# Performance work log

Measured on AMD Instinct MI355X. Metric: run time of the kernel, lower is better.

Reference implementation:

```python
import jax, jax.numpy as jnp
import numpy as np

G, N, F_IN, H, C = 128, 512, 128, 128, 10
LAMB = 1.0
NEG_SLOPE = 0.2
P_EDGE = 32.0 / N  # avg degree ~32


def setup_inputs() -> dict:
    key = jax.random.key(0)
    ks = jax.random.split(key, 12)
    x = jax.random.normal(ks[0], (G, N, F_IN), dtype=jnp.float32)
    # symmetric 0/1 adjacency without self loops (per-graph dense block)
    a = (jax.random.uniform(ks[1], (G, N, N)) < P_EDGE).astype(jnp.float32)
    adj = jnp.maximum(a, jnp.swapaxes(a, 1, 2)) * (1.0 - jnp.eye(N, dtype=jnp.float32))

    def lin(k, fi, fo):
        return (jax.random.normal(k, (fi, fo), dtype=jnp.float32) / np.float32(np.sqrt(fi)))

    return {
        "x": x, "adj": adj,
        "W1": lin(ks[2], F_IN, H), "b1": jnp.zeros((H,), jnp.float32),
        "W2": lin(ks[3], H, H), "b2": jnp.zeros((H,), jnp.float32),
        "W3": lin(ks[4], H, H), "b3": jnp.zeros((H,), jnp.float32),
        "att1_s": 0.1 * jax.random.normal(ks[5], (H,), dtype=jnp.float32),
        "att1_d": 0.1 * jax.random.normal(ks[6], (H,), dtype=jnp.float32),
        "att2_s": 0.1 * jax.random.normal(ks[7], (H,), dtype=jnp.float32),
        "att2_d": 0.1 * jax.random.normal(ks[8], (H,), dtype=jnp.float32),
        "Wl1": lin(ks[9], 2 * H, H), "bl1": jnp.zeros((H,), jnp.float32),
        "Wl2": lin(ks[10], H, H // 2), "bl2": jnp.zeros((H // 2,), jnp.float32),
        "Wl3": lin(ks[11], H // 2, C), "bl3": jnp.zeros((C,), jnp.float32),
    }


def gcn(x, adj, W, b):
    # GCNConv: D^{-1/2} (A + I) D^{-1/2} X W + b  (self-loop weight 1, edge weights in adj)
    deg = adj.sum(-1) + 1.0                              # [G, n]
    dinv = jax.lax.rsqrt(deg)
    xw = x @ W                                           # [G, n, H]
    agg = jnp.einsum('gij,gjf->gif', adj, dinv[..., None] * xw)
    return dinv[..., None] * agg + (dinv * dinv)[..., None] * xw + b


def info_score(x, adj):
    # HGP-SL node information score: row-wise L1 norm of (I - D^{-1} A) X
    deg = jnp.maximum(adj.sum(-1), 1.0)
    agg = jnp.einsum('gij,gjf->gif', adj, x) / deg[..., None]
    return jnp.sum(jnp.abs(x - agg), axis=-1)            # [G, n]


def hgpsl_pool(x, adj, att_s, att_d, k):
    # top-k node selection by information score, then structure learning:
    # dense (sample=False) path: e_ij = leaky_relu(att.[x_i||x_j]) + lamb*A_ij, softmax over j
    s = info_score(x, adj)
    _, idx = jax.lax.top_k(s, k)                         # [G, k]
    xk = jnp.take_along_axis(x, idx[..., None], axis=1)  # [G, k, H]
    g = jnp.arange(x.shape[0])[:, None, None]
    ak = adj[g, idx[:, :, None], idx[:, None, :]]        # induced adjacency [G, k, k]
    e = jax.nn.leaky_relu((xk @ att_s)[:, :, None] + (xk @ att_d)[:, None, :], NEG_SLOPE)
    attn = jax.nn.softmax(e + LAMB * ak, axis=-1)        # new learned edge weights
    return xk, attn


def readout(x):
    # gmp || gap over nodes
    return jnp.concatenate([x.max(axis=1), x.mean(axis=1)], axis=-1)


def reference(x, adj, W1, b1, W2, b2, W3, b3, att1_s, att1_d, att2_s, att2_d,
              Wl1, bl1, Wl2, bl2, Wl3, bl3):
    h = jax.nn.relu(gcn(x, adj, W1, b1))
    h, a1 = hgpsl_pool(h, adj, att1_s, att1_d, N // 2)
    x1 = readout(h)
    h = jax.nn.relu(gcn(h, a1, W2, b2))
    h, a2 = hgpsl_pool(h, a1, att2_s, att2_d, N // 4)
    x2 = readout(h)
    h = jax.nn.relu(gcn(h, a2, W3, b3))
    x3 = readout(h)
    z = jax.nn.relu(x1) + jax.nn.relu(x2) + jax.nn.relu(x3)
    z = jax.nn.relu(z @ Wl1 + bl1)
    z = jax.nn.relu(z @ Wl2 + bl2)
    return jax.nn.softmax(z @ Wl3 + bl3, axis=-1)
```

## Files before the change

### kernel.cpp

```cpp
#include <hip/hip_runtime.h>

#define Gg   128
#define N1   512
#define FH   128
#define K1   256
#define K2   128

typedef __bf16 bf16x8 __attribute__((ext_vector_type(8)));
typedef float  floatx4 __attribute__((ext_vector_type(4)));

__device__ inline float wredsum(float v) {
#pragma unroll
    for (int o = 32; o; o >>= 1) v += __shfl_xor(v, o, 64);
    return v;
}
__device__ inline float wredmax(float v) {
#pragma unroll
    for (int o = 32; o; o >>= 1) v = fmaxf(v, __shfl_xor(v, o, 64));
    return v;
}
__device__ inline unsigned short bf_rne(float x) {
    unsigned u = __float_as_uint(x);
    return (unsigned short)((u + 0x7fffu + ((u >> 16) & 1u)) >> 16);
}
__device__ __forceinline__ void gll16(const void* gsrc, void* lds) {
    __builtin_amdgcn_global_load_lds(
        (const __attribute__((address_space(1))) unsigned int*)gsrc,
        (__attribute__((address_space(3))) unsigned int*)lds, 16, 0, 0);
}

__global__ __launch_bounds__(256) void k_prep_gemm(const float* __restrict__ adj,
        unsigned short* __restrict__ adjbf,
        float* __restrict__ dinv_gcn, float* __restrict__ dinv_info,
        const float* __restrict__ A, const float* __restrict__ W, float* __restrict__ C) {
    __shared__ float Al[64][68];
    __shared__ float Wl[64][132];
    if (blockIdx.x < Gg * N1 / 64) {
        long long row0 = (long long)blockIdx.x * 64;
        int tid = threadIdx.x, tr = tid >> 4, tc = tid & 15;
        float acc[4][8] = {};
        for (int ch = 0; ch < 2; ++ch) {
            for (int p = tid; p < 1024; p += 256) {
                int r = p >> 4, c4 = p & 15;
                *(float4*)&Al[r][c4 * 4] = *(const float4*)(A + (row0 + r) * 128 + ch * 64 + c4 * 4);
            }
            for (int p = tid; p < 2048; p += 256) {
                int r = p >> 5, c4 = p & 31;
                *(float4*)&Wl[r][c4 * 4] = *(const float4*)(W + (ch * 64 + r) * 128 + c4 * 4);
            }
            __syncthreads();
            for (int k = 0; k < 64; ++k) {
                float4 w0 = *(const float4*)&Wl[k][tc * 8];
                float4 w1 = *(const float4*)&Wl[k][tc * 8 + 4];
                float w[8] = {w0.x, w0.y, w0.z, w0.w, w1.x, w1.y, w1.z, w1.w};
#pragma unroll
                for (int i = 0; i < 4; ++i) {
                    float a = Al[tr * 4 + i][k];
#pragma unroll
                    for (int j = 0; j < 8; ++j) acc[i][j] = fmaf(a, w[j], acc[i][j]);
                }
            }
            __syncthreads();
        }
#pragma unroll
        for (int i = 0; i < 4; ++i) {
            long long r = row0 + tr * 4 + i;
            *(float4*)(C + r * 128 + tc * 8)     = make_float4(acc[i][0], acc[i][1], acc[i][2], acc[i][3]);
            *(float4*)(C + r * 128 + tc * 8 + 4) = make_float4(acc[i][4], acc[i][5], acc[i][6], acc[i][7]);
        }
    } else {
        int wave = threadIdx.x >> 6, lane = threadIdx.x & 63;
        long long row = (long long)(blockIdx.x - Gg * N1 / 64) * 4 + wave;
        const float* ar = adj + row * N1;
        float s = 0.f;
        unsigned short ub[8] __attribute__((aligned(16)));
#pragma unroll
        for (int c = 0; c < 2; ++c) {
            float4 v = *(const float4*)(ar + lane * 8 + c * 4);
            s += (v.x + v.y) + (v.z + v.w);
            ub[c * 4 + 0] = (unsigned short)(__float_as_uint(v.x) >> 16);
            ub[c * 4 + 1] = (unsigned short)(__float_as_uint(v.y) >> 16);
            ub[c * 4 + 2] = (unsigned short)(__float_as_uint(v.z) >> 16);
            ub[c * 4 + 3] = (unsigned short)(__float_as_uint(v.w) >> 16);
        }
        *(uint4*)(adjbf + row * N1 + lane * 8) = *(const uint4*)ub;
        s = wredsum(s);
        if (lane == 0) {
            dinv_gcn[row]  = rsqrtf(s + 1.0f);
            dinv_info[row] = 1.0f / fmaxf(s, 1.0f);
        }
    }
}

__global__ __launch_bounds__(256) void k_tsplit(const float* __restrict__ feat,
        const float* __restrict__ rs,
        unsigned short* __restrict__ Thi, unsigned short* __restrict__ Tmid,
        unsigned short* __restrict__ Tlo) {
    __shared__ float tile[64 * 65];
    int b = blockIdx.x;
    int g = b >> 4, rb = (b >> 1) & 7, cb = b & 1;
    int t = threadIdx.x;
    {
        int r0 = t >> 4, c4 = t & 15;
#pragma unroll
        for (int i = 0; i < 4; ++i) {
            int r = r0 + i * 16;
            float4 v = *(const float4*)(feat + ((long long)g * 512 + rb * 64 + r) * 128 + cb * 64 + c4 * 4);
            if (rs) {
                float sc = rs[(long long)g * 512 + rb * 64 + r];
                v.x *= sc; v.y *= sc; v.z *= sc; v.w *= sc;
            }
            tile[r * 65 + c4 * 4 + 0] = v.x;
            tile[r * 65 + c4 * 4 + 1] = v.y;
            tile[r * 65 + c4 * 4 + 2] = v.z;
            tile[r * 65 + c4 * 4 + 3] = v.w;
        }
    }
    __syncthreads();
    int tf = t >> 2, chunk = t & 3;
    unsigned short hbuf[16] __attribute__((aligned(16)));
    unsigned short mbuf[16] __attribute__((aligned(16)));
    unsigned short lbuf[16] __attribute__((aligned(16)));
#pragma unroll
    for (int i = 0; i < 16; ++i) {
        int m = chunk * 16 + i;
        float v = tile[m * 65 + tf];
        unsigned short h = bf_rne(v);
        float fh = __uint_as_float((unsigned)h << 16);
        float r1 = v - fh;
        unsigned short md = bf_rne(r1);
        float fm = __uint_as_float((unsigned)md << 16);
        float r2 = r1 - fm;
        unsigned short lo = bf_rne(r2);
        hbuf[i] = h; mbuf[i] = md; lbuf[i] = lo;
    }
    int sxz = (tf >> 1) & 3;
    int c0 = (chunk & 1) * 2;
    int p0 = (c0 ^ sxz) * 8, p1 = ((c0 + 1) ^ sxz) * 8;
    long long obase = (long long)g * 65536 + (rb * 2 + (chunk >> 1)) * 4096
                    + (cb * 64 + tf) * 32;
    *(uint4*)(Thi + obase + p0)  = *(const uint4*)&hbuf[0];
    *(uint4*)(Thi + obase + p1)  = *(const uint4*)&hbuf[8];
    *(uint4*)(Tmid + obase + p0) = *(const uint4*)&mbuf[0];
    *(uint4*)(Tmid + obase + p1) = *(const uint4*)&mbuf[8];
    *(uint4*)(Tlo + obase + p0)  = *(const uint4*)&lbuf[0];
    *(uint4*)(Tlo + obase + p1)  = *(const uint4*)&lbuf[8];
}

template<int EPI>
__global__ __launch_bounds__(256) void k_aggmm(const unsigned short* __restrict__ adjbf,
        const unsigned short* __restrict__ Bhi, const unsigned short* __restrict__ Bmid,
        const unsigned short* __restrict__ Blo,
        const float* __restrict__ dvec, const float* __restrict__ hx,
        const float* __restrict__ bias, float* __restrict__ outH, float* __restrict__ outS) {
    __shared__ unsigned short Al[2][4096];
    __shared__ unsigned short Blin[2][3][4096];
    __shared__ float sred[2][128];
    int b = blockIdx.x;
    int g  = (b & 7) + ((b >> 5) << 3);
    int rb = (b >> 3) & 3;
    int tid = threadIdx.x;
    int w = tid >> 6, lane = tid & 63;
    int wm = w >> 1, wn = w & 1;
    int ln = lane & 15, quad = lane >> 4;
    int aoff = ((quad ^ ((lane >> 1) & 3)) << 4);
    floatx4 acc[4][4];
#pragma unroll
    for (int i = 0; i < 4; ++i)
#pragma unroll
        for (int j = 0; j < 4; ++j) { floatx4 z = {0.f, 0.f, 0.f, 0.f}; acc[i][j] = z; }

    const char* bsrc0 = (const char*)(Bhi  + (long long)g * 65536);
    const char* bsrc1 = (const char*)(Bmid + (long long)g * 65536);
    const char* bsrc2 = (const char*)(Blo  + (long long)g * 65536);
    int r1 = w * 32 + (lane >> 2);
    int c1 = (lane & 3) ^ ((r1 >> 1) & 3);
    int r2 = r1 + 16;
    int c2 = (lane & 3) ^ ((r2 >> 1) & 3);
    const unsigned short* abase = adjbf + ((long long)g * 512 + rb * 128) * 512;
    const unsigned short* asrc1 = abase + (long long)r1 * 512 + c1 * 8;
    const unsigned short* asrc2 = abase + (long long)r2 * 512 + c2 * 8;

#define STAGE(bi, kkv) do {                                                   \
        char* aldst = (char*)&Al[bi][0] + w * 2048;                           \
        gll16(asrc1 + (kkv), aldst);                                          \
        gll16(asrc2 + (kkv), aldst + 1024);                                   \
        long long soff = (long long)((kkv) >> 5) * 8192 + (w * 2048) + (lane << 4); \
        char* l0 = (char*)&Blin[bi][0][0] + w * 2048;                         \
        char* l1 = (char*)&Blin[bi][1][0] + w * 2048;                         \
        char* l2 = (char*)&Blin[bi][2][0] + w * 2048;                         \
        gll16(bsrc0 + soff,        l0);                                       \
        gll16(bsrc0 + soff + 1024, l0 + 1024);                                \
        gll16(bsrc1 + soff,        l1);                                       \
        gll16(bsrc1 + soff + 1024, l1 + 1024);                                \
        gll16(bsrc2 + soff,        l2);                                       \
        gll16(bsrc2 + soff + 1024, l2 + 1024);                                \
    } while (0)

    STAGE(0, 0);
// ... 7 lines not shown
        }
        __builtin_amdgcn_sched_barrier(0);
        __builtin_amdgcn_s_barrier();
        bf16x8 af[4];
#pragma unroll
        for (int tm = 0; tm < 4; ++tm)
            af[tm] = *(const bf16x8*)((const char*)&Al[cur][0] + (wm * 64 + tm * 16 + ln) * 64 + aoff);
#pragma unroll
        for (int s = 0; s < 3; ++s) {
#pragma unroll
            for (int tn = 0; tn < 4; ++tn) {
                bf16x8 bfr = *(const bf16x8*)((const char*)&Blin[cur][s][0]
                                              + (wn * 64 + tn * 16 + ln) * 64 + aoff);
#pragma unroll
                for (int tm = 0; tm < 4; ++tm)
                    acc[tm][tn] = __builtin_amdgcn_mfma_f32_16x16x32_bf16(af[tm], bfr, acc[tm][tn], 0, 0, 0);
            }
        }
        __builtin_amdgcn_sched_barrier(0);
        __builtin_amdgcn_s_barrier();
    }
#undef STAGE
    long long rowbase = (long long)g * 512 + rb * 128;
    if (EPI == 0) {
#pragma unroll
        for (int tm = 0; tm < 4; ++tm)
#pragma unroll
        for (int r = 0; r < 4; ++r) {
            int ml = wm * 64 + tm * 16 + quad * 4 + r;
            long long grow = rowbase + ml;
            float di = dvec[grow];
#pragma unroll
            for (int tn = 0; tn < 4; ++tn) {
                int nc = wn * 64 + tn * 16 + ln;
                float hv = hx[grow * 128 + nc];
                float o = fmaxf(fmaf(di, acc[tm][tn][r] + di * hv, bias[nc]), 0.f);
                outH[grow * 128 + nc] = o;
            }
        }
    } else {
#pragma unroll
        for (int tm = 0; tm < 4; ++tm)
#pragma unroll
        for (int r = 0; r < 4; ++r) {
            int ml = wm * 64 + tm * 16 + quad * 4 + r;
            long long grow = rowbase + ml;
            float di = dvec[grow];
            float v = 0.f;
#pragma unroll
            for (int tn = 0; tn < 4; ++tn) {
                int nc = wn * 64 + tn * 16 + ln;
                float hv = hx[grow * 128 + nc];
                v += fabsf(hv - acc[tm][tn][r] * di);
            }
            v += __shfl_xor(v, 1); v += __shfl_xor(v, 2);
            v += __shfl_xor(v, 4); v += __shfl_xor(v, 8);
            if (ln == 0) sred[wn][ml] = v;
        }
        __syncthreads();
        if (tid < 128) outS[rowbase + tid] = sred[0][tid] + sred[1][tid];
    }
}

__global__ __launch_bounds__(256) void k_gemm_rw(const float* __restrict__ A,
        const float* __restrict__ W, float* __restrict__ C,
        const float* __restrict__ rs) {
    __shared__ float Al[64][68];
    __shared__ float Wl[64][132];
    long long row0 = (long long)blockIdx.x * 64;
    int tid = threadIdx.x, tr = tid >> 4, tc = tid & 15;
    float acc[4][8] = {};
    for (int ch = 0; ch < 2; ++ch) {
        for (int p = tid; p < 1024; p += 256) {
            int r = p >> 4, c4 = p & 15;
            *(float4*)&Al[r][c4 * 4] = *(const float4*)(A + (row0 + r) * 128 + ch * 64 + c4 * 4);
        }
        for (int p = tid; p < 2048; p += 256) {
            int r = p >> 5, c4 = p & 31;
            *(float4*)&Wl[r][c4 * 4] = *(const float4*)(W + (ch * 64 + r) * 128 + c4 * 4);
        }
        __syncthreads();
        for (int k = 0; k < 64; ++k) {
            float4 w0 = *(const float4*)&Wl[k][tc * 8];
            float4 w1 = *(const float4*)&Wl[k][tc * 8 + 4];
            float w[8] = {w0.x, w0.y, w0.z, w0.w, w1.x, w1.y, w1.z, w1.w};
#pragma unroll
            for (int i = 0; i < 4; ++i) {
                float a = Al[tr * 4 + i][k];
#pragma unroll
                for (int j = 0; j < 8; ++j) acc[i][j] = fmaf(a, w[j], acc[i][j]);
            }
        }
        __syncthreads();
    }
#pragma unroll
    for (int i = 0; i < 4; ++i) {
        long long r = row0 + tr * 4 + i;
        float sc = rs ? rs[r] : 1.0f;
        *(float4*)(C + r * 128 + tc * 8)     = make_float4(sc * acc[i][0], sc * acc[i][1], sc * acc[i][2], sc * acc[i][3]);
        *(float4*)(C + r * 128 + tc * 8 + 4) = make_float4(sc * acc[i][4], sc * acc[i][5], sc * acc[i][6], sc * acc[i][7]);
    }
}

template<int NT, int KSEL>
__global__ __launch_bounds__(256) void k_topk(const float* __restrict__ s, int* __restrict__ idx) {
    __shared__ unsigned long long keys[NT];
    int g = blockIdx.x;
    const float* sg = s + g * NT;
    for (int t = threadIdx.x; t < NT; t += 256) {
        unsigned int b = __float_as_uint(sg[t]);
        unsigned int ord = (b & 0x80000000u) ? ~b : (b | 0x80000000u);
        keys[t] = ((unsigned long long)(~ord) << 32) | (unsigned int)t;
    }
    __syncthreads();
    for (int k = 2; k <= NT; k <<= 1) {
        for (int j = k >> 1; j > 0; j >>= 1) {
            for (int i = threadIdx.x; i < NT; i += 256) {
                int l = i ^ j;
                if (l > i) {
                    bool dir = ((i & k) == 0);
                    unsigned long long a = keys[i], b2 = keys[l];
                    bool sw = dir ? (a > b2) : (a < b2);
                    if (sw) { keys[i] = b2; keys[l] = a; }
                }
            }
            __syncthreads();
        }
    }
    for (int t = threadIdx.x; t < KSEL; t += 256)
        idx[g * KSEL + t] = (int)(keys[t] & 0xffffffffu);
}

template<int KK>
__global__ __launch_bounds__(256) void k_gather(const float* __restrict__ h, int srcN,
        const int* __restrict__ idx, const float* __restrict__ atts, const float* __restrict__ attd,
        float* __restrict__ xk, float* __restrict__ as_, float* __restrict__ ad_) {
    int wave = threadIdx.x >> 6, lane = threadIdx.x & 63;
    int r = blockIdx.x * 4 + wave;
    int g = r / KK;
    int j = idx[r];
    float2 v = *(const float2*)(h + ((long long)g * srcN + j) * 128 + lane * 2);
    *(float2*)(xk + (long long)r * 128 + lane * 2) = v;
    float2 sv = *(const float2*)(atts + lane * 2);
    float2 dv = *(const float2*)(attd + lane * 2);
    float ps = v.x * sv.x + v.y * sv.y;
    float pd = v.x * dv.x + v.y * dv.y;
    ps = wredsum(ps); pd = wredsum(pd);
    if (lane == 0) { as_[r] = ps; ad_[r] = pd; }
}

template<int KK, int SRCN, bool BF16>
__global__ __launch_bounds__(256) void k_attnro(const void* __restrict__ adjSrc,
        const int* __restrict__ idx, const float* __restrict__ as_, const float* __restrict__ ad_,
        float* __restrict__ attn, float* __restrict__ dgo, float* __restrict__ dio,
        const float* __restrict__ xk, float* __restrict__ xo) {
    constexpr int E = KK / 64;
// ... 6 lines not shown
        if (t < 128) {
            const float* p = xk + (long long)g * KK * 128 + t;
            float m = -1e30f, s = 0.f;
            for (int r = 0; r < KK; ++r) { float v = p[r * 128]; m = fmaxf(m, v); s += v; }
            xo[g * 256 + t] = m;
            xo[g * 256 + 128 + t] = s * (1.0f / KK);
        }
        return;
    }
    int bpg = KK / 4;
    int g = blockIdx.x / bpg;
    int wave = threadIdx.x >> 6, lane = threadIdx.x & 63;
    int i = (blockIdx.x % bpg) * 4 + wave;
    for (int t = threadIdx.x; t < KK; t += 256) { idxL[t] = idx[g * KK + t]; adL[t] = ad_[g * KK + t]; }
    __syncthreads();
    int ri = idxL[i];
    if (BF16) {
        const unsigned short* arow = (const unsigned short*)adjSrc + ((long long)g * SRCN + ri) * SRCN;
        for (int c = lane; c < SRCN; c += 64)
            rowL[wave][c] = __uint_as_float((unsigned)arow[c] << 16);
    } else {
        const float* arow = (const float*)adjSrc + ((long long)g * SRCN + ri) * SRCN;
        for (int c = lane; c < SRCN; c += 64) rowL[wave][c] = arow[c];
    }
    float asi = as_[g * KK + i];
    float vals[E];
    float m = -1e30f;
#pragma unroll
    for (int e = 0; e < E; ++e) {
        int j = e * 64 + lane;
        float x = asi + adL[j];
        x = (x >= 0.f) ? x : 0.2f * x;
        x += rowL[wave][idxL[j]];
        vals[e] = x; m = fmaxf(m, x);
    }
    m = wredmax(m);
    float S = 0.f;
#pragma unroll
    for (int e = 0; e < E; ++e) { vals[e] = expf(vals[e] - m); S += vals[e]; }
    S = wredsum(S);
    float inv = 1.f / S, rs = 0.f;
    float* orow = attn + ((long long)g * KK + i) * KK;
#pragma unroll
    for (int e = 0; e < E; ++e) { float p = vals[e] * inv; rs += p; orow[e * 64 + lane] = p; }
    rs = wredsum(rs);
    if (lane == 0) { dgo[g * KK + i] = rsqrtf(rs + 1.f); dio[g * KK + i] = 1.f / fmaxf(rs, 1.f); }
}

template<int KK, bool SCALEY, int EPI>
__global__ __launch_bounds__(256) void k_agg(const float* __restrict__ A, const float* __restrict__ Y,
        const float* __restrict__ dg, const float* __restrict__ di_,
        const float* __restrict__ bias, const float* __restrict__ hx,
        float* __restrict__ outH, float* __restrict__ outS) {
    __shared__ float Al[64][68];
    __shared__ float Yl[64][132];
    __shared__ float red[64][17];
    constexpr int RB = KK / 64;
    int g = blockIdx.x / RB;
    int rb = blockIdx.x % RB;
    const float* Ag = A + (long long)g * KK * KK;
    const float* Yg = Y + (long long)g * KK * 128;
    int tid = threadIdx.x, tr = tid >> 4, tc = tid & 15;
    float acc[4][8] = {};
    for (int ch = 0; ch < KK / 64; ++ch) {
        for (int p = tid; p < 1024; p += 256) {
            int r = p >> 4, c4 = p & 15;
            *(float4*)&Al[r][c4 * 4] = *(const float4*)(Ag + (rb * 64 + r) * KK + ch * 64 + c4 * 4);
        }
        for (int p = tid; p < 2048; p += 256) {
            int r = p >> 5, c4 = p & 31;
            float4 v = *(const float4*)(Yg + (ch * 64 + r) * 128 + c4 * 4);
            if (SCALEY) { float sc = dg[g * KK + ch * 64 + r]; v.x *= sc; v.y *= sc; v.z *= sc; v.w *= sc; }
            *(float4*)&Yl[r][c4 * 4] = v;
        }
        __syncthreads();
        for (int k = 0; k < 64; ++k) {
            float4 w0 = *(const float4*)&Yl[k][tc * 8];
            float4 w1 = *(const float4*)&Yl[k][tc * 8 + 4];
            float w[8] = {w0.x, w0.y, w0.z, w0.w, w1.x, w1.y, w1.z, w1.w};
#pragma unroll
            for (int i = 0; i < 4; ++i) {
                float a = Al[tr * 4 + i][k];
#pragma unroll
                for (int j = 0; j < 8; ++j) acc[i][j] = fmaf(a, w[j], acc[i][j]);
            }
        }
        __syncthreads();
    }
    int i0 = rb * 64 + tr * 4;
    if (EPI == 0) {
#pragma unroll
        for (int i = 0; i < 4; ++i) {
            long long gi = (long long)g * KK + i0 + i;
            float d = dg[gi], dd = d * d;
            float4 x0 = *(const float4*)(hx + gi * 128 + tc * 8);
            float4 x1 = *(const float4*)(hx + gi * 128 + tc * 8 + 4);
            float4 b0 = *(const float4*)(bias + tc * 8);
            float4 b1 = *(const float4*)(bias + tc * 8 + 4);
            float4 o0, o1;
            o0.x = fmaxf(fmaf(d, acc[i][0], fmaf(dd, x0.x, b0.x)), 0.f);
            o0.y = fmaxf(fmaf(d, acc[i][1], fmaf(dd, x0.y, b0.y)), 0.f);
            o0.z = fmaxf(fmaf(d, acc[i][2], fmaf(dd, x0.z, b0.z)), 0.f);
            o0.w = fmaxf(fmaf(d, acc[i][3], fmaf(dd, x0.w, b0.w)), 0.f);
            o1.x = fmaxf(fmaf(d, acc[i][4], fmaf(dd, x1.x, b1.x)), 0.f);
            o1.y = fmaxf(fmaf(d, acc[i][5], fmaf(dd, x1.y, b1.y)), 0.f);
            o1.z = fmaxf(fmaf(d, acc[i][6], fmaf(dd, x1.z, b1.z)), 0.f);
            o1.w = fmaxf(fmaf(d, acc[i][7], fmaf(dd, x1.w, b1.w)), 0.f);
            *(float4*)(outH + gi * 128 + tc * 8)     = o0;
            *(float4*)(outH + gi * 128 + tc * 8 + 4) = o1;
        }
    } else {
#pragma unroll
        for (int i = 0; i < 4; ++i) {
            long long gi = (long long)g * KK + i0 + i;
            float d = di_[gi];
            float4 x0 = *(const float4*)(hx + gi * 128 + tc * 8);
            float4 x1 = *(const float4*)(hx + gi * 128 + tc * 8 + 4);
            float p = fabsf(x0.x - acc[i][0] * d) + fabsf(x0.y - acc[i][1] * d)
                    + fabsf(x0.z - acc[i][2] * d) + fabsf(x0.w - acc[i][3] * d)
                    + fabsf(x1.x - acc[i][4] * d) + fabsf(x1.y - acc[i][5] * d)
                    + fabsf(x1.z - acc[i][6] * d) + fabsf(x1.w - acc[i][7] * d);
            red[tr * 4 + i][tc] = p;
        }
        __syncthreads();
        if (tid < 64) {
            float s = 0.f;
#pragma unroll
            for (int t = 0; t < 16; ++t) s += red[tid][t];
            outS[(long long)g * KK + rb * 64 + tid] = s;
        }
    }
}

__global__ __launch_bounds__(128) void k_mlp(const float* __restrict__ x1, const float* __restrict__ x2,
        const float* __restrict__ h3,
        const float* __restrict__ Wl1, const float* __restrict__ bl1,
        const float* __restrict__ Wl2, const float* __restrict__ bl2,
        const float* __restrict__ Wl3, const float* __restrict__ bl3,
        float* __restrict__ out) {
    __shared__ float z[256], z1[128], z2[64], lg[10];
    int g = blockIdx.x, t = threadIdx.x;
    {
        const float* p = h3 + (long long)g * K2 * 128 + t;
        float m = -1e30f, s = 0.f;
        for (int r = 0; r < K2; ++r) { float v = p[r * 128]; m = fmaxf(m, v); s += v; }
        float x3a = m, x3b = s * (1.0f / K2);
        z[t]       = fmaxf(x1[g * 256 + t], 0.f)       + fmaxf(x2[g * 256 + t], 0.f)       + fmaxf(x3a, 0.f);
        z[t + 128] = fmaxf(x1[g * 256 + 128 + t], 0.f) + fmaxf(x2[g * 256 + 128 + t], 0.f) + fmaxf(x3b, 0.f);
    }
    __syncthreads();
    {
        float acc = bl1[t];
        for (int k = 0; k < 256; ++k) acc = fmaf(z[k], Wl1[k * 128 + t], acc);
        z1[t] = fmaxf(acc, 0.f);
    }
    __syncthreads();
    if (t < 64) {
        float acc = bl2[t];
        for (int k = 0; k < 128; ++k) acc = fmaf(z1[k], Wl2[k * 64 + t], acc);
        z2[t] = fmaxf(acc, 0.f);
    }
    __syncthreads();
    if (t < 10) {
        float acc = bl3[t];
        for (int k = 0; k < 64; ++k) acc = fmaf(z2[k], Wl3[k * 10 + t], acc);
        lg[t] = acc;
    }
    __syncthreads();
    if (t == 0) {
        float m = -1e30f;
        for (int c = 0; c < 10; ++c) m = fmaxf(m, lg[c]);
        float S = 0.f;
        float e[10];
        for (int c = 0; c < 10; ++c) { e[c] = expf(lg[c] - m); S += e[c]; }
        float inv = 1.f / S;
        for (int c = 0; c < 10; ++c) out[g * 10 + c] = e[c] * inv;
    }
}

extern "C" void kernel_launch(void* const* d_in, const int* in_sizes, int n_in,
                              void* d_out, int out_size, void* d_ws, size_t ws_size,
                              hipStream_t stream) {
    const float* x     = (const float*)d_in[0];
    const float* adj   = (const float*)d_in[1];
    const float* W1    = (const float*)d_in[2];
    const float* b1    = (const float*)d_in[3];
    const float* W2    = (const float*)d_in[4];
    const float* b2    = (const float*)d_in[5];
    const float* W3    = (const float*)d_in[6];
    const float* b3    = (const float*)d_in[7];
    const float* att1s = (const float*)d_in[8];
    const float* att1d = (const float*)d_in[9];
    const float* att2s = (const float*)d_in[10];
    const float* att2d = (const float*)d_in[11];
    const float* Wl1   = (const float*)d_in[12];
    const float* bl1   = (const float*)d_in[13];
    const float* Wl2   = (const float*)d_in[14];
    const float* bl2   = (const float*)d_in[15];
    const float* Wl3   = (const float*)d_in[16];
    const float* bl3   = (const float*)d_in[17];
    float* out = (float*)d_out;

    char* ws = (char*)d_ws;
    unsigned short* Thi  = (unsigned short*)(ws + 0);
    unsigned short* Tmid = (unsigned short*)(ws + 16777216);
    unsigned short* Tlo  = (unsigned short*)(ws + 33554432);
    float* xk1 = (float*)(ws + 0);
    float* xw2 = (float*)(ws + 16777216);
    float* h2  = (float*)(ws + 33554432);
    float* xk2 = (float*)(ws + 16777216);
    float* a2  = (float*)(ws + 25165824);
    float* xw3 = (float*)(ws + 0);
    float* h3  = (float*)(ws + 8388608);
    float* dxw1 = (float*)(ws + 50331648);
    float* h1   = dxw1;
    float* a1   = dxw1;
    float* s1      = (float*)(ws + 83886080);
    int*   idx1    = (int*)  (ws + 84148224);
    float* as1     = (float*)(ws + 84279296);
    float* ad1     = (float*)(ws + 84410368);
    float* dinv_g1 = (float*)(ws + 84541440);
    float* dinv_i1 = (float*)(ws + 84803584);
    float* dinv_g2 = (float*)(ws + 85065728);
    float* dinv_i2 = (float*)(ws + 85196800);
    float* x1r     = (float*)(ws + 85327872);
    float* s2      = (float*)(ws + 85458944);
    int*   idx2    = (int*)  (ws + 85590016);
    float* as2     = (float*)(ws + 85655552);
    float* ad2     = (float*)(ws + 85721088);
    float* dinv_g3 = (float*)(ws + 85786624);
    float* dinv_i3 = (float*)(ws + 85852160);
    float* x2r     = (float*)(ws + 85917696);
    unsigned short* adjbf = (unsigned short*)(ws + 100663296);

    k_prep_gemm<<<Gg * N1 / 64 + Gg * N1 / 4, 256, 0, stream>>>(adj, adjbf, dinv_g1, dinv_i1, x, W1, dxw1);
    k_tsplit<<<Gg * 16, 256, 0, stream>>>(dxw1, dinv_g1, Thi, Tmid, Tlo);
    k_aggmm<0><<<Gg * 4, 256, 0, stream>>>(adjbf, Thi, Tmid, Tlo, dinv_g1, dxw1, b1, h1, nullptr);
    k_tsplit<<<Gg * 16, 256, 0, stream>>>(h1, nullptr, Thi, Tmid, Tlo);
    k_aggmm<1><<<Gg * 4, 256, 0, stream>>>(adjbf, Thi, Tmid, Tlo, dinv_i1, h1, nullptr, nullptr, s1);
    k_topk<N1, K1><<<Gg, 256, 0, stream>>>(s1, idx1);
    k_gather<K1><<<Gg * K1 / 4, 256, 0, stream>>>(h1, N1, idx1, att1s, att1d, xk1, as1, ad1);
    k_attnro<K1, N1, true><<<Gg * K1 / 4 + Gg, 256, 0, stream>>>(adjbf, idx1, as1, ad1, a1, dinv_g2, dinv_i2, xk1, x1r);

    k_gemm_rw<<<Gg * K1 / 64, 256, 0, stream>>>(xk1, W2, xw2, nullptr);
    k_agg<K1, true, 0><<<Gg * (K1 / 64), 256, 0, stream>>>(a1, xw2, dinv_g2, dinv_i2, b2, xw2, h2, nullptr);
    k_agg<K1, false, 1><<<Gg * (K1 / 64), 256, 0, stream>>>(a1, h2, dinv_g2, dinv_i2, b2, h2, nullptr, s2);
    k_topk<K1, K2><<<Gg, 256, 0, stream>>>(s2, idx2);
    k_gather<K2><<<Gg * K2 / 4, 256, 0, stream>>>(h2, K1, idx2, att2s, att2d, xk2, as2, ad2);
    k_attnro<K2, K1, false><<<Gg * K2 / 4 + Gg, 256, 0, stream>>>(a1, idx2, as2, ad2, a2, dinv_g3, dinv_i3, xk2, x2r);

    k_gemm_rw<<<Gg * K2 / 64, 256, 0, stream>>>(xk2, W3, xw3, nullptr);
    k_agg<K2, true, 0><<<Gg * (K2 / 64), 256, 0, stream>>>(a2, xw3, dinv_g3, dinv_i3, b3, xw3, h3, nullptr);

    k_mlp<<<Gg, 128, 0, stream>>>(x1r, x2r, h3, Wl1, bl1, Wl2, bl2, Wl3, bl3, out);
}
```

Baseline: 580.4 us.

## Enlarge fp32 GEMM tiles to 128 rows with 8x8 per-thread blocking

The fp32 dense GEMM and aggregation kernels now compute 128-row tiles with an 8x8 register block per thread. The A tile is stored transposed in LDS so each thread can read its A values as float4 vectors. This raises FMA work per LDS load and halves the number of blocks. The first-layer GEMM is split out of the fused prep kernel into its own launch. The cost is higher register pressure, fewer blocks (as few as 128 for some launches), transposed-store LDS bank conflicts, and one extra kernel launch.

```diff
diff --git a/kernel.cpp b/kernel.cpp
--- a/kernel.cpp
+++ b/kernel.cpp
@@ -29,66 +29,73 @@
         (__attribute__((address_space(3))) unsigned int*)lds, 16, 0, 0);
 }
 
-__global__ __launch_bounds__(256) void k_prep_gemm(const float* __restrict__ adj,
+__global__ __launch_bounds__(256) void k_prep(const float* __restrict__ adj,
         unsigned short* __restrict__ adjbf,
-        float* __restrict__ dinv_gcn, float* __restrict__ dinv_info,
-        const float* __restrict__ A, const float* __restrict__ W, float* __restrict__ C) {
-    __shared__ float Al[64][68];
+        float* __restrict__ dinv_gcn, float* __restrict__ dinv_info) {
+    int wave = threadIdx.x >> 6, lane = threadIdx.x & 63;
+    long long row = (long long)blockIdx.x * 4 + wave;
+    const float* ar = adj + row * N1;
+    float s = 0.f;
+    unsigned short ub[8] __attribute__((aligned(16)));
+#pragma unroll
+    for (int c = 0; c < 2; ++c) {
+        float4 v = *(const float4*)(ar + lane * 8 + c * 4);
+        s += (v.x + v.y) + (v.z + v.w);
+        ub[c * 4 + 0] = (unsigned short)(__float_as_uint(v.x) >> 16);
+        ub[c * 4 + 1] = (unsigned short)(__float_as_uint(v.y) >> 16);
+        ub[c * 4 + 2] = (unsigned short)(__float_as_uint(v.z) >> 16);
+        ub[c * 4 + 3] = (unsigned short)(__float_as_uint(v.w) >> 16);
+    }
+    *(uint4*)(adjbf + row * N1 + lane * 8) = *(const uint4*)ub;
+    s = wredsum(s);
+    if (lane == 0) {
+        dinv_gcn[row]  = rsqrtf(s + 1.0f);
+        dinv_info[row] = 1.0f / fmaxf(s, 1.0f);
+    }
+}
+
+__global__ __launch_bounds__(256) void k_gemm_rw(const float* __restrict__ A,
+        const float* __restrict__ W, float* __restrict__ C,
+        const float* __restrict__ rs) {
+    __shared__ float Alt[64][132];
     __shared__ float Wl[64][132];
-    if (blockIdx.x < Gg * N1 / 64) {
-        long long row0 = (long long)blockIdx.x * 64;
-        int tid = threadIdx.x, tr = tid >> 4, tc = tid & 15;
-        float acc[4][8] = {};
-        for (int ch = 0; ch < 2; ++ch) {
-            for (int p = tid; p < 1024; p += 256) {
-                int r = p >> 4, c4 = p & 15;
-                *(float4*)&Al[r][c4 * 4] = *(const float4*)(A + (row0 + r) * 128 + ch * 64 + c4 * 4);
-            }
-            for (int p = tid; p < 2048; p += 256) {
-                int r = p >> 5, c4 = p & 31;
-                *(float4*)&Wl[r][c4 * 4] = *(const float4*)(W + (ch * 64 + r) * 128 + c4 * 4);
-            }
-            __syncthreads();
-            for (int k = 0; k < 64; ++k) {
-                float4 w0 = *(const float4*)&Wl[k][tc * 8];
-                float4 w1 = *(const float4*)&Wl[k][tc * 8 + 4];
-                float w[8] = {w0.x, w0.y, w0.z, w0.w, w1.x, w1.y, w1.z, w1.w};
-#pragma unroll
-                for (int i = 0; i < 4; ++i) {
-                    float a = Al[tr * 4 + i][k];
-#pragma unroll
-                    for (int j = 0; j < 8; ++j) acc[i][j] = fmaf(a, w[j], acc[i][j]);
-                }
-            }
-            __syncthreads();
-        }
-#pragma unroll
-        for (int i = 0; i < 4; ++i) {
-            long long r = row0 + tr * 4 + i;
-            *(float4*)(C + r * 128 + tc * 8)     = make_float4(acc[i][0], acc[i][1], acc[i][2], acc[i][3]);
-            *(float4*)(C + r * 128 + tc * 8 + 4) = make_float4(acc[i][4], acc[i][5], acc[i][6], acc[i][7]);
-        }
-    } else {
-        int wave = threadIdx.x >> 6, lane = threadIdx.x & 63;
-        long long row = (long long)(blockIdx.x - Gg * N1 / 64) * 4 + wave;
-        const float* ar = adj + row * N1;
-        float s = 0.f;
-        unsigned short ub[8] __attribute__((aligned(16)));
-#pragma unroll
-        for (int c = 0; c < 2; ++c) {
-            float4 v = *(const float4*)(ar + lane * 8 + c * 4);
-            s += (v.x + v.y) + (v.z + v.w);
-            ub[c * 4 + 0] = (unsigned short)(__float_as_uint(v.x) >> 16);
-            ub[c * 4 + 1] = (unsigned short)(__float_as_uint(v.y) >> 16);
-            ub[c * 4 + 2] = (unsigned short)(__float_as_uint(v.z) >> 16);
-            ub[c * 4 + 3] = (unsigned short)(__float_as_uint(v.w) >> 16);
-        }
-        *(uint4*)(adjbf + row * N1 + lane * 8) = *(const uint4*)ub;
-        s = wredsum(s);
-        if (lane == 0) {
-            dinv_gcn[row]  = rsqrtf(s + 1.0f);
-            dinv_info[row] = 1.0f / fmaxf(s, 1.0f);
-        }
+    long long row0 = (long long)blockIdx.x * 128;
+    int tid = threadIdx.x, tr = tid >> 4, tc = tid & 15;
+    float acc[8][8] = {};
+    for (int ch = 0; ch < 2; ++ch) {
+        for (int p = tid; p < 2048; p += 256) {
+            int r = p >> 4, c4 = p & 15;
+            float4 v = *(const float4*)(A + (row0 + r) * 128 + ch * 64 + c4 * 4);
+            Alt[c4 * 4 + 0][r] = v.x;
+            Alt[c4 * 4 + 1][r] = v.y;
+            Alt[c4 * 4 + 2][r] = v.z;
+            Alt[c4 * 4 + 3][r] = v.w;
+        }
+        for (int p = tid; p < 2048; p += 256) {
+            int r = p >> 5, c4 = p & 31;
+            *(float4*)&Wl[r][c4 * 4] = *(const float4*)(W + (ch * 64 + r) * 128 + c4 * 4);
+        }
+        __syncthreads();
+        for (int k = 0; k < 64; ++k) {
+            float4 a0 = *(const float4*)&Alt[k][tr * 8];
+            float4 a1 = *(const float4*)&Alt[k][tr * 8 + 4];
+            float4 w0 = *(const float4*)&Wl[k][tc * 8];
+            float4 w1 = *(const float4*)&Wl[k][tc * 8 + 4];
+            float a[8] = {a0.x, a0.y, a0.z, a0.w, a1.x, a1.y, a1.z, a1.w};
+            float w[8] = {w0.x, w0.y, w0.z, w0.w, w1.x, w1.y, w1.z, w1.w};
+#pragma unroll
+            for (int i = 0; i < 8; ++i)
+#pragma unroll
+                for (int j = 0; j < 8; ++j) acc[i][j] = fmaf(a[i], w[j], acc[i][j]);
+        }
+        __syncthreads();
+    }
+#pragma unroll
+    for (int i = 0; i < 8; ++i) {
+        long long r = row0 + tr * 8 + i;
+        float sc = rs ? rs[r] : 1.0f;
+        *(float4*)(C + r * 128 + tc * 8)     = make_float4(sc * acc[i][0], sc * acc[i][1], sc * acc[i][2], sc * acc[i][3]);
+        *(float4*)(C + r * 128 + tc * 8 + 4) = make_float4(sc * acc[i][4], sc * acc[i][5], sc * acc[i][6], sc * acc[i][7]);
     }
 }
 
@@ -268,46 +275,6 @@
     }
 }
 
-__global__ __launch_bounds__(256) void k_gemm_rw(const float* __restrict__ A,
-        const float* __restrict__ W, float* __restrict__ C,
-        const float* __restrict__ rs) {
-    __shared__ float Al[64][68];
-    __shared__ float Wl[64][132];
-    long long row0 = (long long)blockIdx.x * 64;
-    int tid = threadIdx.x, tr = tid >> 4, tc = tid & 15;
-    float acc[4][8] = {};
-    for (int ch = 0; ch < 2; ++ch) {
-        for (int p = tid; p < 1024; p += 256) {
-            int r = p >> 4, c4 = p & 15;
-            *(float4*)&Al[r][c4 * 4] = *(const float4*)(A + (row0 + r) * 128 + ch * 64 + c4 * 4);
-        }
-        for (int p = tid; p < 2048; p += 256) {
-            int r = p >> 5, c4 = p & 31;
-            *(float4*)&Wl[r][c4 * 4] = *(const float4*)(W + (ch * 64 + r) * 128 + c4 * 4);
-        }
-        __syncthreads();
-        for (int k = 0; k < 64; ++k) {
-            float4 w0 = *(const float4*)&Wl[k][tc * 8];
-            float4 w1 = *(const float4*)&Wl[k][tc * 8 + 4];
-            float w[8] = {w0.x, w0.y, w0.z, w0.w, w1.x, w1.y, w1.z, w1.w};
-#pragma unroll
-            for (int i = 0; i < 4; ++i) {
-                float a = Al[tr * 4 + i][k];
-#pragma unroll
-                for (int j = 0; j < 8; ++j) acc[i][j] = fmaf(a, w[j], acc[i][j]);
-            }
-        }
-        __syncthreads();
-    }
-#pragma unroll
-    for (int i = 0; i < 4; ++i) {
-        long long r = row0 + tr * 4 + i;
-        float sc = rs ? rs[r] : 1.0f;
-        *(float4*)(C + r * 128 + tc * 8)     = make_float4(sc * acc[i][0], sc * acc[i][1], sc * acc[i][2], sc * acc[i][3]);
-        *(float4*)(C + r * 128 + tc * 8 + 4) = make_float4(sc * acc[i][4], sc * acc[i][5], sc * acc[i][6], sc * acc[i][7]);
-    }
-}
-
 template<int NT, int KSEL>
 __global__ __launch_bounds__(256) void k_topk(const float* __restrict__ s, int* __restrict__ idx) {
     __shared__ unsigned long long keys[NT];
@@ -420,20 +387,23 @@
         const float* __restrict__ dg, const float* __restrict__ di_,
         const float* __restrict__ bias, const float* __restrict__ hx,
         float* __restrict__ outH, float* __restrict__ outS) {
-    __shared__ float Al[64][68];
+    __shared__ float Alt[64][132];
     __shared__ float Yl[64][132];
-    __shared__ float red[64][17];
-    constexpr int RB = KK / 64;
+    constexpr int RB = KK / 128;
     int g = blockIdx.x / RB;
     int rb = blockIdx.x % RB;
     const float* Ag = A + (long long)g * KK * KK;
     const float* Yg = Y + (long long)g * KK * 128;
     int tid = threadIdx.x, tr = tid >> 4, tc = tid & 15;
-    float acc[4][8] = {};
+    float acc[8][8] = {};
     for (int ch = 0; ch < KK / 64; ++ch) {
-        for (int p = tid; p < 1024; p += 256) {
+        for (int p = tid; p < 2048; p += 256) {
             int r = p >> 4, c4 = p & 15;
-            *(float4*)&Al[r][c4 * 4] = *(const float4*)(Ag + (rb * 64 + r) * KK + ch * 64 + c4 * 4);
+            float4 v = *(const float4*)(Ag + (long long)(rb * 128 + r) * KK + ch * 64 + c4 * 4);
+            Alt[c4 * 4 + 0][r] = v.x;
+            Alt[c4 * 4 + 1][r] = v.y;
+            Alt[c4 * 4 + 2][r] = v.z;
+            Alt[c4 * 4 + 3][r] = v.w;
         }
         for (int p = tid; p < 2048; p += 256) {
             int r = p >> 5, c4 = p & 31;
@@ -443,22 +413,23 @@
         }
         __syncthreads();
         for (int k = 0; k < 64; ++k) {
+            float4 a0 = *(const float4*)&Alt[k][tr * 8];
+            float4 a1 = *(const float4*)&Alt[k][tr * 8 + 4];
             float4 w0 = *(const float4*)&Yl[k][tc * 8];
             float4 w1 = *(const float4*)&Yl[k][tc * 8 + 4];
+            float a[8] = {a0.x, a0.y, a0.z, a0.w, a1.x, a1.y, a1.z, a1.w};
             float w[8] = {w0.x, w0.y, w0.z, w0.w, w1.x, w1.y, w1.z, w1.w};
 #pragma unroll
-            for (int i = 0; i < 4; ++i) {
-                float a = Al[tr * 4 + i][k];
-#pragma unroll
-                for (int j = 0; j < 8; ++j) acc[i][j] = fmaf(a, w[j], acc[i][j]);
-            }
+            for (int i = 0; i < 8; ++i)
+#pragma unroll
+                for (int j = 0; j < 8; ++j) acc[i][j] = fmaf(a[i], w[j], acc[i][j]);
         }
         __syncthreads();
     }
-    int i0 = rb * 64 + tr * 4;
+    int i0 = rb * 128 + tr * 8;
     if (EPI == 0) {
 #pragma unroll
-        for (int i = 0; i < 4; ++i) {
+        for (int i = 0; i < 8; ++i) {
             long long gi = (long long)g * KK + i0 + i;
             float d = dg[gi], dd = d * d;
             float4 x0 = *(const float4*)(hx + gi * 128 + tc * 8);
@@ -478,8 +449,9 @@
             *(float4*)(outH + gi * 128 + tc * 8 + 4) = o1;
         }
     } else {
-#pragma unroll
-        for (int i = 0; i < 4; ++i) {
+        float* red = &Alt[0][0];
+#pragma unroll
+        for (int i = 0; i < 8; ++i) {
             long long gi = (long long)g * KK + i0 + i;
             float d = di_[gi];
             float4 x0 = *(const float4*)(hx + gi * 128 + tc * 8);
@@ -488,14 +460,14 @@
                     + fabsf(x0.z - acc[i][2] * d) + fabsf(x0.w - acc[i][3] * d)
                     + fabsf(x1.x - acc[i][4] * d) + fabsf(x1.y - acc[i][5] * d)
                     + fabsf(x1.z - acc[i][6] * d) + fabsf(x1.w - acc[i][7] * d);
-            red[tr * 4 + i][tc] = p;
+            red[(tr * 8 + i) * 17 + tc] = p;
         }
         __syncthreads();
-        if (tid < 64) {
+        if (tid < 128) {
             float s = 0.f;
 #pragma unroll
-            for (int t = 0; t < 16; ++t) s += red[tid][t];
-            outS[(long long)g * KK + rb * 64 + tid] = s;
+            for (int t = 0; t < 16; ++t) s += red[tid * 17 + t];
+            outS[(long long)g * KK + rb * 128 + tid] = s;
         }
     }
 }
@@ -601,7 +573,8 @@
     float* x2r     = (float*)(ws + 85917696);
     unsigned short* adjbf = (unsigned short*)(ws + 100663296);
 
-    k_prep_gemm<<<Gg * N1 / 64 + Gg * N1 / 4, 256, 0, stream>>>(adj, adjbf, dinv_g1, dinv_i1, x, W1, dxw1);
+    k_gemm_rw<<<Gg * N1 / 128, 256, 0, stream>>>(x, W1, dxw1, nullptr);
+    k_prep<<<Gg * N1 / 4, 256, 0, stream>>>(adj, adjbf, dinv_g1, dinv_i1);
     k_tsplit<<<Gg * 16, 256, 0, stream>>>(dxw1, dinv_g1, Thi, Tmid, Tlo);
     k_aggmm<0><<<Gg * 4, 256, 0, stream>>>(adjbf, Thi, Tmid, Tlo, dinv_g1, dxw1, b1, h1, nullptr);
     k_tsplit<<<Gg * 16, 256, 0, stream>>>(h1, nullptr, Thi, Tmid, Tlo);
@@ -610,15 +583,15 @@
     k_gather<K1><<<Gg * K1 / 4, 256, 0, stream>>>(h1, N1, idx1, att1s, att1d, xk1, as1, ad1);
     k_attnro<K1, N1, true><<<Gg * K1 / 4 + Gg, 256, 0, stream>>>(adjbf, idx1, as1, ad1, a1, dinv_g2, dinv_i2, xk1, x1r);
 
-    k_gemm_rw<<<Gg * K1 / 64, 256, 0, stream>>>(xk1, W2, xw2, nullptr);
-    k_agg<K1, true, 0><<<Gg * (K1 / 64), 256, 0, stream>>>(a1, xw2, dinv_g2, dinv_i2, b2, xw2, h2, nullptr);
-    k_agg<K1, false, 1><<<Gg * (K1 / 64), 256, 0, stream>>>(a1, h2, dinv_g2, dinv_i2, b2, h2, nullptr, s2);
+    k_gemm_rw<<<Gg * K1 / 128, 256, 0, stream>>>(xk1, W2, xw2, nullptr);
+    k_agg<K1, true, 0><<<Gg * (K1 / 128), 256, 0, stream>>>(a1, xw2, dinv_g2, dinv_i2, b2, xw2, h2, nullptr);
+    k_agg<K1, false, 1><<<Gg * (K1 / 128), 256, 0, stream>>>(a1, h2, dinv_g2, dinv_i2, b2, h2, nullptr, s2);
     k_topk<K1, K2><<<Gg, 256, 0, stream>>>(s2, idx2);
     k_gather<K2><<<Gg * K2 / 4, 256, 0, stream>>>(h2, K1, idx2, att2s, att2d, xk2, as2, ad2);
     k_attnro<K2, K1, false><<<Gg * K2 / 4 + Gg, 256, 0, stream>>>(a1, idx2, as2, ad2, a2, dinv_g3, dinv_i3, xk2, x2r);
 
-    k_gemm_rw<<<Gg * K2 / 64, 256, 0, stream>>>(xk2, W3, xw3, nullptr);
-    k_agg<K2, true, 0><<<Gg * (K2 / 64), 256, 0, stream>>>(a2, xw3, dinv_g3, dinv_i3, b3, xw3, h3, nullptr);
+    k_gemm_rw<<<Gg * K2 / 128, 256, 0, stream>>>(xk2, W3, xw3, nullptr);
+    k_agg<K2, true, 0><<<Gg * (K2 / 128), 256, 0, stream>>>(a2, xw3, dinv_g3, dinv_i3, b3, xw3, h3, nullptr);
 
     k_mlp<<<Gg, 128, 0, stream>>>(x1r, x2r, h3, Wl1, bl1, Wl2, bl2, Wl3, bl3, out);
 }
```

After: 622.9 us. 1.07x slower.

## Use split-bf16 MFMA for level-2 aggregation instead of fp32 aggregation kernels

Applied to the files above, without the earlier changes.

Replaces the two level-2 k_agg calls, the GCN aggregation and the info-score aggregation over the 256-node learned adjacency, with MFMA bf16 GEMMs. The dense attention matrix and the feature matrix are each split into three bf16 parts (hi/mid/lo) and combined with six cross-product MFMAs, which keeps near-fp32 accuracy. This adds split kernels and extra global traffic for the split buffers, and moves the aggregation onto matrix cores. Separately, the first GEMM in k_prep_gemm now stages K in 32-wide chunks instead of 64, which shrinks its LDS footprint.

```diff
diff --git a/kernel.cpp b/kernel.cpp
--- a/kernel.cpp
+++ b/kernel.cpp
@@ -14,14 +14,14 @@
     for (int o = 32; o; o >>= 1) v += __shfl_xor(v, o, 64);
     return v;
 }
-__device__ inline float wredmax(float v) {
-#pragma unroll
-    for (int o = 32; o; o >>= 1) v = fmaxf(v, __shfl_xor(v, o, 64));
-    return v;
-}
 __device__ inline unsigned short bf_rne(float x) {
     unsigned u = __float_as_uint(x);
     return (unsigned short)((u + 0x7fffu + ((u >> 16) & 1u)) >> 16);
+}
+__device__ inline float wredmax(float v) {
+#pragma unroll
+    for (int o = 32; o; o >>= 1) v = fmaxf(v, __shfl_xor(v, o, 64));
+    return v;
 }
 __device__ __forceinline__ void gll16(const void* gsrc, void* lds) {
     __builtin_amdgcn_global_load_lds(
@@ -33,23 +33,23 @@
         unsigned short* __restrict__ adjbf,
         float* __restrict__ dinv_gcn, float* __restrict__ dinv_info,
         const float* __restrict__ A, const float* __restrict__ W, float* __restrict__ C) {
-    __shared__ float Al[64][68];
-    __shared__ float Wl[64][132];
+    __shared__ float Al[64][36];
+    __shared__ float Wl[32][132];
     if (blockIdx.x < Gg * N1 / 64) {
         long long row0 = (long long)blockIdx.x * 64;
         int tid = threadIdx.x, tr = tid >> 4, tc = tid & 15;
         float acc[4][8] = {};
-        for (int ch = 0; ch < 2; ++ch) {
+        for (int ch = 0; ch < 4; ++ch) {
+            for (int p = tid; p < 512; p += 256) {
+                int r = p >> 3, c4 = p & 7;
+                *(float4*)&Al[r][c4 * 4] = *(const float4*)(A + (row0 + r) * 128 + ch * 32 + c4 * 4);
+            }
             for (int p = tid; p < 1024; p += 256) {
-                int r = p >> 4, c4 = p & 15;
-                *(float4*)&Al[r][c4 * 4] = *(const float4*)(A + (row0 + r) * 128 + ch * 64 + c4 * 4);
-            }
-            for (int p = tid; p < 2048; p += 256) {
                 int r = p >> 5, c4 = p & 31;
-                *(float4*)&Wl[r][c4 * 4] = *(const float4*)(W + (ch * 64 + r) * 128 + c4 * 4);
+                *(float4*)&Wl[r][c4 * 4] = *(const float4*)(W + (ch * 32 + r) * 128 + c4 * 4);
             }
             __syncthreads();
-            for (int k = 0; k < 64; ++k) {
+            for (int k = 0; k < 32; ++k) {
                 float4 w0 = *(const float4*)&Wl[k][tc * 8];
                 float4 w1 = *(const float4*)&Wl[k][tc * 8 + 4];
                 float w[8] = {w0.x, w0.y, w0.z, w0.w, w1.x, w1.y, w1.z, w1.w};
@@ -145,6 +145,87 @@
     *(uint4*)(Tmid + obase + p1) = *(const uint4*)&mbuf[8];
     *(uint4*)(Tlo + obase + p0)  = *(const uint4*)&lbuf[0];
     *(uint4*)(Tlo + obase + p1)  = *(const uint4*)&lbuf[8];
+}
+
+__global__ __launch_bounds__(256) void k_fsplit256(const float* __restrict__ feat,
+        const float* __restrict__ rs,
+        unsigned short* __restrict__ Thi, unsigned short* __restrict__ Tmid,
+        unsigned short* __restrict__ Tlo) {
+    __shared__ float tile[64 * 65];
+    int b = blockIdx.x;
+    int g = b >> 3, rb = (b >> 1) & 3, cb = b & 1;
+    int t = threadIdx.x;
+    {
+        int r0 = t >> 4, c4 = t & 15;
+#pragma unroll
+        for (int i = 0; i < 4; ++i) {
+            int r = r0 + i * 16;
+            float4 v = *(const float4*)(feat + ((long long)g * 256 + rb * 64 + r) * 128 + cb * 64 + c4 * 4);
+            if (rs) {
+                float sc = rs[(long long)g * 256 + rb * 64 + r];
+                v.x *= sc; v.y *= sc; v.z *= sc; v.w *= sc;
+            }
+            tile[r * 65 + c4 * 4 + 0] = v.x;
+            tile[r * 65 + c4 * 4 + 1] = v.y;
+            tile[r * 65 + c4 * 4 + 2] = v.z;
+            tile[r * 65 + c4 * 4 + 3] = v.w;
+        }
+    }
+    __syncthreads();
+    int tf = t >> 2, chunk = t & 3;
+    unsigned short hbuf[16] __attribute__((aligned(16)));
+    unsigned short mbuf[16] __attribute__((aligned(16)));
+    unsigned short lbuf[16] __attribute__((aligned(16)));
+#pragma unroll
+    for (int i = 0; i < 16; ++i) {
+        int m = chunk * 16 + i;
+        float v = tile[m * 65 + tf];
+        unsigned short h = bf_rne(v);
+        float fh = __uint_as_float((unsigned)h << 16);
+        float r1 = v - fh;
+        unsigned short md = bf_rne(r1);
+        float fm = __uint_as_float((unsigned)md << 16);
+        float r2 = r1 - fm;
+        unsigned short lo = bf_rne(r2);
+        hbuf[i] = h; mbuf[i] = md; lbuf[i] = lo;
+    }
+    int sxz = (tf >> 1) & 3;
+    int c0 = (chunk & 1) * 2;
+    int p0 = (c0 ^ sxz) * 8, p1 = ((c0 + 1) ^ sxz) * 8;
+    long long obase = (long long)g * 32768 + (rb * 2 + (chunk >> 1)) * 4096
+                    + (cb * 64 + tf) * 32;
+    *(uint4*)(Thi + obase + p0)  = *(const uint4*)&hbuf[0];
+    *(uint4*)(Thi + obase + p1)  = *(const uint4*)&hbuf[8];
+    *(uint4*)(Tmid + obase + p0) = *(const uint4*)&mbuf[0];
+    *(uint4*)(Tmid + obase + p1) = *(const uint4*)&mbuf[8];
+    *(uint4*)(Tlo + obase + p0)  = *(const uint4*)&lbuf[0];
+    *(uint4*)(Tlo + obase + p1)  = *(const uint4*)&lbuf[8];
+}
+
+__global__ __launch_bounds__(256) void k_asplit(const float* __restrict__ a,
+        unsigned short* __restrict__ aH, unsigned short* __restrict__ aM,
+        unsigned short* __restrict__ aL) {
+    long long i4 = ((long long)blockIdx.x * 256 + threadIdx.x) * 4;
+    float4 v = *(const float4*)(a + i4);
+    ushort4 h, m, l;
+    float vv[4] = {v.x, v.y, v.z, v.w};
+    unsigned short hb[4], mb[4], lb[4];
+#pragma unroll
+    for (int i = 0; i < 4; ++i) {
+        unsigned short hh = bf_rne(vv[i]);
+        float fh = __uint_as_float((unsigned)hh << 16);
+        float r1 = vv[i] - fh;
+        unsigned short mm = bf_rne(r1);
+        float fm = __uint_as_float((unsigned)mm << 16);
+        unsigned short ll = bf_rne(r1 - fm);
+        hb[i] = hh; mb[i] = mm; lb[i] = ll;
+    }
+    h = make_ushort4(hb[0], hb[1], hb[2], hb[3]);
+    m = make_ushort4(mb[0], mb[1], mb[2], mb[3]);
+    l = make_ushort4(lb[0], lb[1], lb[2], lb[3]);
+    *(ushort4*)(aH + i4) = h;
+    *(ushort4*)(aM + i4) = m;
+    *(ushort4*)(aL + i4) = l;
 }
 
 template<int EPI>
@@ -258,6 +339,138 @@
                 int nc = wn * 64 + tn * 16 + ln;
                 float hv = hx[grow * 128 + nc];
                 v += fabsf(hv - acc[tm][tn][r] * di);
+            }
+            v += __shfl_xor(v, 1); v += __shfl_xor(v, 2);
+            v += __shfl_xor(v, 4); v += __shfl_xor(v, 8);
+            if (ln == 0) sred[wn][ml] = v;
+        }
+        __syncthreads();
+        if (tid < 128) outS[rowbase + tid] = sred[0][tid] + sred[1][tid];
+    }
+}
+
+template<int EPI>
+__global__ __launch_bounds__(256) void k_aggmm2(
+        const unsigned short* __restrict__ aH, const unsigned short* __restrict__ aM,
+        const unsigned short* __restrict__ aL,
+        const unsigned short* __restrict__ bH, const unsigned short* __restrict__ bM,
+        const unsigned short* __restrict__ bL,
+        const float* __restrict__ dvec, const float* __restrict__ hx,
+        const float* __restrict__ bias, float* __restrict__ outH, float* __restrict__ outS) {
+    __shared__ unsigned short As[2][3][4096];
+    __shared__ unsigned short Bs[2][3][4096];
+    __shared__ float sred[2][128];
+    int b = blockIdx.x;
+    int g = b >> 1, rb = b & 1;
+    int tid = threadIdx.x;
+    int w = tid >> 6, lane = tid & 63;
+    int wm = w >> 1, wn = w & 1;
+    int ln = lane & 15, quad = lane >> 4;
+    int aoff = ((quad ^ ((lane >> 1) & 3)) << 4);
+    floatx4 acc[4][4];
+#pragma unroll
+    for (int i = 0; i < 4; ++i)
+#pragma unroll
+        for (int j = 0; j < 4; ++j) { floatx4 z = {0.f, 0.f, 0.f, 0.f}; acc[i][j] = z; }
+
+    int r1 = w * 32 + (lane >> 2);
+    int c1 = (lane & 3) ^ ((r1 >> 1) & 3);
+    int r2 = r1 + 16;
+    int c2 = (lane & 3) ^ ((r2 >> 1) & 3);
+    long long arow0 = ((long long)g * 256 + rb * 128);
+    const unsigned short* ah1 = aH + (arow0 + r1) * 256 + c1 * 8;
+    const unsigned short* ah2 = aH + (arow0 + r2) * 256 + c2 * 8;
+    const unsigned short* am1 = aM + (arow0 + r1) * 256 + c1 * 8;
+    const unsigned short* am2 = aM + (arow0 + r2) * 256 + c2 * 8;
+    const unsigned short* al1 = aL + (arow0 + r1) * 256 + c1 * 8;
+    const unsigned short* al2 = aL + (arow0 + r2) * 256 + c2 * 8;
+    const char* bb0 = (const char*)(bH + (long long)g * 32768);
+    const char* bb1 = (const char*)(bM + (long long)g * 32768);
+    const char* bb2 = (const char*)(bL + (long long)g * 32768);
+
+#define STAGE2(bi, kkv) do {                                                  \
+        char* ad0 = (char*)&As[bi][0][0] + w * 2048;                          \
+        char* ad1 = (char*)&As[bi][1][0] + w * 2048;                          \
+        char* ad2 = (char*)&As[bi][2][0] + w * 2048;                          \
+        gll16(ah1 + (kkv), ad0);  gll16(ah2 + (kkv), ad0 + 1024);             \
+        gll16(am1 + (kkv), ad1);  gll16(am2 + (kkv), ad1 + 1024);             \
+        gll16(al1 + (kkv), ad2);  gll16(al2 + (kkv), ad2 + 1024);             \
+        long long soff = (long long)((kkv) >> 5) * 8192 + (w * 2048) + (lane << 4); \
+        char* l0 = (char*)&Bs[bi][0][0] + w * 2048;                           \
+        char* l1 = (char*)&Bs[bi][1][0] + w * 2048;                           \
+        char* l2 = (char*)&Bs[bi][2][0] + w * 2048;                           \
+        gll16(bb0 + soff,        l0);  gll16(bb0 + soff + 1024, l0 + 1024);   \
+        gll16(bb1 + soff,        l1);  gll16(bb1 + soff + 1024, l1 + 1024);   \
+        gll16(bb2 + soff,        l2);  gll16(bb2 + soff + 1024, l2 + 1024);   \
+    } while (0)
+
+    STAGE2(0, 0);
+    for (int kk = 0; kk < 256; kk += 32) {
+        int cur = (kk >> 5) & 1;
+        if (kk + 32 < 256) {
+            STAGE2(cur ^ 1, kk + 32);
+            asm volatile("s_waitcnt vmcnt(12)" ::: "memory");
+        } else {
+            asm volatile("s_waitcnt vmcnt(0)" ::: "memory");
+        }
+        __builtin_amdgcn_sched_barrier(0);
+        __builtin_amdgcn_s_barrier();
+        bf16x8 af[3][4];
+#pragma unroll
+        for (int s = 0; s < 3; ++s)
+#pragma unroll
+        for (int tm = 0; tm < 4; ++tm)
+            af[s][tm] = *(const bf16x8*)((const char*)&As[cur][s][0] + (wm * 64 + tm * 16 + ln) * 64 + aoff);
+#pragma unroll
+        for (int tn = 0; tn < 4; ++tn) {
+            bf16x8 bh = *(const bf16x8*)((const char*)&Bs[cur][0][0] + (wn * 64 + tn * 16 + ln) * 64 + aoff);
+            bf16x8 bm = *(const bf16x8*)((const char*)&Bs[cur][1][0] + (wn * 64 + tn * 16 + ln) * 64 + aoff);
+            bf16x8 bl = *(const bf16x8*)((const char*)&Bs[cur][2][0] + (wn * 64 + tn * 16 + ln) * 64 + aoff);
+#pragma unroll
+            for (int tm = 0; tm < 4; ++tm) {
+                acc[tm][tn] = __builtin_amdgcn_mfma_f32_16x16x32_bf16(af[0][tm], bh, acc[tm][tn], 0, 0, 0);
+                acc[tm][tn] = __builtin_amdgcn_mfma_f32_16x16x32_bf16(af[0][tm], bm, acc[tm][tn], 0, 0, 0);
+                acc[tm][tn] = __builtin_amdgcn_mfma_f32_16x16x32_bf16(af[1][tm], bh, acc[tm][tn], 0, 0, 0);
+                acc[tm][tn] = __builtin_amdgcn_mfma_f32_16x16x32_bf16(af[0][tm], bl, acc[tm][tn], 0, 0, 0);
+                acc[tm][tn] = __builtin_amdgcn_mfma_f32_16x16x32_bf16(af[1][tm], bm, acc[tm][tn], 0, 0, 0);
+                acc[tm][tn] = __builtin_amdgcn_mfma_f32_16x16x32_bf16(af[2][tm], bh, acc[tm][tn], 0, 0, 0);
+            }
+        }
+        __builtin_amdgcn_sched_barrier(0);
+        __builtin_amdgcn_s_barrier();
+    }
+#undef STAGE2
+    long long rowbase = (long long)g * 256 + rb * 128;
+    if (EPI == 0) {
+#pragma unroll
+        for (int tm = 0; tm < 4; ++tm)
+#pragma unroll
+        for (int r = 0; r < 4; ++r) {
+            int ml = wm * 64 + tm * 16 + quad * 4 + r;
+            long long grow = rowbase + ml;
+            float d = dvec[grow], dd = d * d;
+#pragma unroll
+            for (int tn = 0; tn < 4; ++tn) {
+                int nc = wn * 64 + tn * 16 + ln;
+                float hv = hx[grow * 128 + nc];
+                float o = fmaxf(fmaf(d, acc[tm][tn][r], fmaf(dd, hv, bias[nc])), 0.f);
+                outH[grow * 128 + nc] = o;
+            }
+        }
+    } else {
+#pragma unroll
+        for (int tm = 0; tm < 4; ++tm)
+#pragma unroll
+        for (int r = 0; r < 4; ++r) {
+            int ml = wm * 64 + tm * 16 + quad * 4 + r;
+            long long grow = rowbase + ml;
+            float d = dvec[grow];
+            float v = 0.f;
+#pragma unroll
+            for (int tn = 0; tn < 4; ++tn) {
+                int nc = wn * 64 + tn * 16 + ln;
+                float hv = hx[grow * 128 + nc];
+                v += fabsf(hv - acc[tm][tn][r] * d);
             }
             v += __shfl_xor(v, 1); v += __shfl_xor(v, 2);
             v += __shfl_xor(v, 4); v += __shfl_xor(v, 8);
@@ -600,6 +813,12 @@
     float* dinv_i3 = (float*)(ws + 85852160);
     float* x2r     = (float*)(ws + 85917696);
     unsigned short* adjbf = (unsigned short*)(ws + 100663296);
+    unsigned short* aSh = (unsigned short*)(ws + 176160768);
+    unsigned short* aSm = (unsigned short*)(ws + 192937984);
+    unsigned short* aSl = (unsigned short*)(ws + 209715200);
+    unsigned short* bSh = (unsigned short*)(ws + 226492416);
+    unsigned short* bSm = (unsigned short*)(ws + 234881024);
+    unsigned short* bSl = (unsigned short*)(ws + 243269632);
 
     k_prep_gemm<<<Gg * N1 / 64 + Gg * N1 / 4, 256, 0, stream>>>(adj, adjbf, dinv_g1, dinv_i1, x, W1, dxw1);
     k_tsplit<<<Gg * 16, 256, 0, stream>>>(dxw1, dinv_g1, Thi, Tmid, Tlo);
@@ -611,8 +830,11 @@
     k_attnro<K1, N1, true><<<Gg * K1 / 4 + Gg, 256, 0, stream>>>(adjbf, idx1, as1, ad1, a1, dinv_g2, dinv_i2, xk1, x1r);
 
     k_gemm_rw<<<Gg * K1 / 64, 256, 0, stream>>>(xk1, W2, xw2, nullptr);
-    k_agg<K1, true, 0><<<Gg * (K1 / 64), 256, 0, stream>>>(a1, xw2, dinv_g2, dinv_i2, b2, xw2, h2, nullptr);
-    k_agg<K1, false, 1><<<Gg * (K1 / 64), 256, 0, stream>>>(a1, h2, dinv_g2, dinv_i2, b2, h2, nullptr, s2);
+    k_asplit<<<Gg * K1 * K1 / 1024, 256, 0, stream>>>(a1, aSh, aSm, aSl);
+    k_fsplit256<<<Gg * 8, 256, 0, stream>>>(xw2, dinv_g2, bSh, bSm, bSl);
+    k_aggmm2<0><<<Gg * 2, 256, 0, stream>>>(aSh, aSm, aSl, bSh, bSm, bSl, dinv_g2, xw2, b2, h2, nullptr);
+    k_fsplit256<<<Gg * 8, 256, 0, stream>>>(h2, nullptr, bSh, bSm, bSl);
+    k_aggmm2<1><<<Gg * 2, 256, 0, stream>>>(aSh, aSm, aSl, bSh, bSm, bSl, dinv_i2, h2, nullptr, nullptr, s2);
     k_topk<K1, K2><<<Gg, 256, 0, stream>>>(s2, idx2);
     k_gather<K2><<<Gg * K2 / 4, 256, 0, stream>>>(h2, K1, idx2, att2s, att2d, xk2, as2, ad2);
     k_attnro<K2, K1, false><<<Gg * K2 / 4 + Gg, 256, 0, stream>>>(a1, idx2, as2, ad2, a2, dinv_g3, dinv_i3, xk2, x2r);
```

Result: no change. 591.6 us (+1.9%).
